# Kernel optimization log

Measured on AMD Instinct MI355X. Metric: run time of the kernel, lower is better.

Reference implementation:

```python
import jax, jax.numpy as jnp
import numpy as np

BITS = 4
PACK = 32 // BITS  # 8 nibbles per int32
MASK = (1 << BITS) - 1  # 0xF, maxq for 4-bit


def _unpack_rows(q):
    # q: [K//PACK, N] int32, nibbles packed along the input (row) dim
    shifts = (jnp.arange(PACK, dtype=jnp.int32) * BITS)
    vals = (q[:, None, :] >> shifts[None, :, None]) & MASK  # [K//PACK, PACK, N]
    return vals.reshape(q.shape[0] * PACK, q.shape[1])      # [K, N]


def _unpack_cols(q):
    # q: [1, N//PACK] int32, nibbles packed along the output (col) dim
    shifts = (jnp.arange(PACK, dtype=jnp.int32) * BITS)
    vals = (q[:, :, None] >> shifts[None, None, :]) & MASK  # [1, N//PACK, PACK]
    return vals.reshape(q.shape[0], q.shape[1] * PACK)       # [1, N]


def setup_inputs() -> dict:
    key = jax.random.key(0)
    k1, k2, k3, k4 = jax.random.split(key, 4)
    M, K, N = 4096, 4096, 11008
    x = jax.random.normal(k1, (M, K), dtype=jnp.float16)
    qweight = jax.random.randint(k2, (K // PACK, N), jnp.iinfo(jnp.int32).min,
                                 jnp.iinfo(jnp.int32).max, dtype=jnp.int32)
    qzeros = jax.random.randint(k3, (1, N // PACK), jnp.iinfo(jnp.int32).min,
                                jnp.iinfo(jnp.int32).max, dtype=jnp.int32)
    # realistic small positive per-channel scales
    scales = (jax.random.uniform(k4, (1, N), dtype=jnp.float32) * 0.01 + 1e-3).astype(jnp.float16)
    return {"x": x, "qweight": qweight, "qzeros": qzeros, "scales": scales}


def reference(x, qweight, qzeros, scales):
    # GPTQ/exllama 4-bit dequant: w = scale * (q - (zero + 1)), single group
    wq = _unpack_rows(qweight)                      # [K, N] int32 in [0, 15]
    zeros = _unpack_cols(qzeros) + 1                # [1, N] int32
    w = (wq - zeros).astype(jnp.float16) * scales   # [K, N] fp16
    out = jnp.dot(x, w)                             # [M, N] fp16 GEMM
    return out
```

## Files before the change

kernel.cpp:

```cpp
#include <hip/hip_runtime.h>
#include <stdint.h>

#define M_DIM 4096
#define K_DIM 4096
#define N_DIM 11008

typedef _Float16 half2v __attribute__((ext_vector_type(2)));
typedef _Float16 half8  __attribute__((ext_vector_type(8)));
typedef float    f32x4  __attribute__((ext_vector_type(4)));

__device__ __forceinline__ unsigned int pkrtz_bits(float a, float b) {
  typedef __fp16 fp16x2 __attribute__((ext_vector_type(2)));
  union { fp16x2 h; unsigned int u; } c;
  c.h = __builtin_amdgcn_cvt_pkrtz(a, b);
  return c.u;
}

__device__ __forceinline__ half8 pack8(float4 lo, float4 hi) {
  union { unsigned int u[4]; half8 v; } r;
  r.u[0] = pkrtz_bits(lo.x, hi.x);
  r.u[1] = pkrtz_bits(lo.y, hi.y);
  r.u[2] = pkrtz_bits(lo.z, hi.z);
  r.u[3] = pkrtz_bits(lo.w, hi.w);
  return r.v;
}

__global__ __launch_bounds__(256) void convert_x(const float* __restrict__ X,
                                                 _Float16* __restrict__ X16) {
  size_t g = (size_t)blockIdx.x * 256 + threadIdx.x;
  const float4* p = (const float4*)(X + g * 8);
  float4 lo = p[0], hi = p[1];
  *(half8*)(X16 + g * 8) = pack8(lo, hi);
}

__device__ __forceinline__ half8 unpack8(unsigned int q, half2v zoff) {
  union { unsigned int u; half2v h; } t0, t1, t2, t3;
  t0.u = (q & 0x000F000Fu) | 0x64006400u;
  t1.u = ((q >> 4) & 0x000F000Fu) | 0x64006400u;
  t2.u = ((q >> 8) & 0x000F000Fu) | 0x64006400u;
  t3.u = ((q >> 12) & 0x000F000Fu) | 0x64006400u;
  union { half2v h[4]; half8 v; } r;
  r.h[0] = t0.h - zoff;
  r.h[1] = t1.h - zoff;
  r.h[2] = t2.h - zoff;
  r.h[3] = t3.h - zoff;
  return r.v;
}

__device__ __forceinline__ void stage16(const void* g, void* l) {
  __builtin_amdgcn_global_load_lds((__attribute__((address_space(1))) unsigned int*)g,
                                   (__attribute__((address_space(3))) unsigned int*)l,
                                   16, 0, 0);
}

__global__ __launch_bounds__(256, 3) void gptq_gemm(
    const _Float16* __restrict__ X16,
    const int* __restrict__ QW,
    const int* __restrict__ QZ,
    const float* __restrict__ SC,
    float* __restrict__ OUT) {
  const int tid  = threadIdx.x;
  const int lane = tid & 63;
  const int wave = tid >> 6;
  const int wr   = wave >> 1;
  const int wc   = wave & 1;
  const int quad = lane >> 4;
  const int l16  = lane & 15;
  const int bx = blockIdx.x;
  const int by = blockIdx.y;

  __shared__ __align__(16) _Float16 ldsA[2 * 1024 * 8];

  const _Float16* gA = X16 + (size_t)(by * 128 + (tid & 127)) * K_DIM + (tid >> 7) * 8;
  _Float16* lA = ldsA + (size_t)tid * 8;

  const int* qp = QW + (size_t)quad * N_DIM + bx * 128 + wc * 64 + l16;

  half2v zoff[4];
  float sc[4];
#pragma unroll
  for (int nt = 0; nt < 4; ++nt) {
    int n = bx * 128 + wc * 64 + nt * 16 + l16;
    int z = (QZ[n >> 3] >> ((n & 7) * 4)) & 15;
    union { unsigned int u; half2v h; } zc;
    unsigned int zb = 0x6400u + (unsigned int)(z + 1);
    zc.u = (zb << 16) | zb;
    zoff[nt] = zc.h;
    sc[nt] = SC[n];
  }

  f32x4 acc[4][4] = {};

#pragma unroll
  for (int i = 0; i < 4; ++i)
    stage16(gA + i * 16, lA + i * 2048);
  int q[2][4];
#pragma unroll
  for (int s = 0; s < 2; ++s)
#pragma unroll
    for (int nt = 0; nt < 4; ++nt)
      q[s][nt] = qp[(s * 4) * N_DIM + nt * 16];
  __syncthreads();

  int p = 0;
  for (int ks = 0; ks < 64; ++ks) {
    int nq[2][4];
    if (ks < 63) {
      gA += 64;
      qp += 8 * N_DIM;
      _Float16* lb = ldsA + (p ^ 1) * 8192 + (size_t)tid * 8;
#pragma unroll
      for (int i = 0; i < 4; ++i)
        stage16(gA + i * 16, lb + i * 2048);
#pragma unroll
      for (int s = 0; s < 2; ++s)
#pragma unroll
        for (int nt = 0; nt < 4; ++nt)
          nq[s][nt] = qp[(s * 4) * N_DIM + nt * 16];
    }

    const _Float16* base = ldsA + p * 8192;
#pragma unroll
    for (int s = 0; s < 2; ++s) {
      half8 a[4];
#pragma unroll
      for (int mt = 0; mt < 4; ++mt)
        a[mt] = *(const half8*)(base + ((s * 4 + quad) * 128 + wr * 64 + mt * 16 + l16) * 8);
      half8 b[4];
#pragma unroll
      for (int nt = 0; nt < 4; ++nt)
        b[nt] = unpack8((unsigned int)q[s][nt], zoff[nt]);
#pragma unroll
      for (int mt = 0; mt < 4; ++mt)
#pragma unroll
        for (int nt = 0; nt < 4; ++nt)
          acc[mt][nt] = __builtin_amdgcn_mfma_f32_16x16x32_f16(a[mt], b[nt], acc[mt][nt], 0, 0, 0);
    }
    __syncthreads();
    if (ks < 63) {
#pragma unroll
      for (int s = 0; s < 2; ++s)
#pragma unroll
        for (int nt = 0; nt < 4; ++nt)
          q[s][nt] = nq[s][nt];
    }
    p ^= 1;
  }

#pragma unroll
  for (int mt = 0; mt < 4; ++mt) {
    int mbase = by * 128 + wr * 64 + mt * 16 + quad * 4;
#pragma unroll
    for (int nt = 0; nt < 4; ++nt) {
      int n = bx * 128 + wc * 64 + nt * 16 + l16;
      float s = sc[nt];
#pragma unroll
      for (int pp = 0; pp < 4; ++pp)
        OUT[(size_t)(mbase + pp) * N_DIM + n] = acc[mt][nt][pp] * s;
    }
  }
}

extern "C" void kernel_launch(void* const* d_in, const int* in_sizes, int n_in,
                              void* d_out, int out_size, void* d_ws, size_t ws_size,
                              hipStream_t stream) {
  const float* X  = (const float*)d_in[0];
  const int* QW   = (const int*)d_in[1];
  const int* QZ   = (const int*)d_in[2];
  const float* SC = (const float*)d_in[3];
  float* OUT      = (float*)d_out;
  _Float16* X16   = (_Float16*)d_ws;

  convert_x<<<dim3((M_DIM * (size_t)K_DIM / 8) / 256), 256, 0, stream>>>(X, X16);
  dim3 grid(N_DIM / 128, M_DIM / 128);
  gptq_gemm<<<grid, 256, 0, stream>>>(X16, QW, QZ, SC, OUT);
}
```

Before: 662.2 us.

## Triple-buffer A tiles in LDS with partial vmcnt waits and MFMA priority

Moves from a double-buffered LDS pipeline to three buffers with prefetch depth two. Each iteration issues loads for A and qweight two stages ahead, then waits with a partial s_waitcnt vmcnt(12) before a raw s_barrier instead of a full __syncthreads drain, so global loads stay in flight across iterations. It also raises wave priority around the MFMA block and adds sched_barrier fences to pin the instruction order. This adds LDS use (48KB per block, which may cut occupancy from 3 blocks per CU) and more live registers. The hand-counted vmcnt must match the actual number of outstanding loads, or the kernel will read stale data.

```diff
diff --git a/kernel.cpp b/kernel.cpp
--- a/kernel.cpp
+++ b/kernel.cpp
@@ -8,6 +8,8 @@
 typedef _Float16 half2v __attribute__((ext_vector_type(2)));
 typedef _Float16 half8  __attribute__((ext_vector_type(8)));
 typedef float    f32x4  __attribute__((ext_vector_type(4)));
+
+#define SCHED_FENCE() __builtin_amdgcn_sched_barrier(0)
 
 __device__ __forceinline__ unsigned int pkrtz_bits(float a, float b) {
   typedef __fp16 fp16x2 __attribute__((ext_vector_type(2)));
@@ -69,10 +71,10 @@
   const int bx = blockIdx.x;
   const int by = blockIdx.y;
 
-  __shared__ __align__(16) _Float16 ldsA[2 * 1024 * 8];
+  __shared__ __align__(16) _Float16 ldsA[3 * 1024 * 8];
 
   const _Float16* gA = X16 + (size_t)(by * 128 + (tid & 127)) * K_DIM + (tid >> 7) * 8;
-  _Float16* lA = ldsA + (size_t)tid * 8;
+  _Float16* lw = ldsA + (size_t)tid * 8;
 
   const int* qp = QW + (size_t)quad * N_DIM + bx * 128 + wc * 64 + l16;
 
@@ -91,24 +93,40 @@
 
   f32x4 acc[4][4] = {};
 
+  int q0[2][4], q1[2][4];
 #pragma unroll
   for (int i = 0; i < 4; ++i)
-    stage16(gA + i * 16, lA + i * 2048);
-  int q[2][4];
+    stage16(gA + i * 16, lw + i * 2048);
+  SCHED_FENCE();
 #pragma unroll
   for (int s = 0; s < 2; ++s)
 #pragma unroll
     for (int nt = 0; nt < 4; ++nt)
-      q[s][nt] = qp[(s * 4) * N_DIM + nt * 16];
-  __syncthreads();
-
-  int p = 0;
+      q0[s][nt] = qp[(s * 4) * N_DIM + nt * 16];
+  SCHED_FENCE();
+  gA += 64;
+  qp += 8 * N_DIM;
+#pragma unroll
+  for (int i = 0; i < 4; ++i)
+    stage16(gA + i * 16, lw + 8192 + i * 2048);
+  SCHED_FENCE();
+#pragma unroll
+  for (int s = 0; s < 2; ++s)
+#pragma unroll
+    for (int nt = 0; nt < 4; ++nt)
+      q1[s][nt] = qp[(s * 4) * N_DIM + nt * 16];
+  SCHED_FENCE();
+  asm volatile("s_waitcnt vmcnt(12)" ::: "memory");
+  __builtin_amdgcn_s_barrier();
+
+  int rb = 0;
+  int wb = 2;
   for (int ks = 0; ks < 64; ++ks) {
     int nq[2][4];
-    if (ks < 63) {
+    if (ks < 62) {
       gA += 64;
       qp += 8 * N_DIM;
-      _Float16* lb = ldsA + (p ^ 1) * 8192 + (size_t)tid * 8;
+      _Float16* lb = ldsA + wb * 8192 + (size_t)tid * 8;
 #pragma unroll
       for (int i = 0; i < 4; ++i)
         stage16(gA + i * 16, lb + i * 2048);
@@ -117,9 +135,10 @@
 #pragma unroll
         for (int nt = 0; nt < 4; ++nt)
           nq[s][nt] = qp[(s * 4) * N_DIM + nt * 16];
-    }
-
-    const _Float16* base = ldsA + p * 8192;
+      SCHED_FENCE();
+    }
+
+    const _Float16* base = ldsA + rb * 8192;
 #pragma unroll
     for (int s = 0; s < 2; ++s) {
       half8 a[4];
@@ -129,22 +148,34 @@
       half8 b[4];
 #pragma unroll
       for (int nt = 0; nt < 4; ++nt)
-        b[nt] = unpack8((unsigned int)q[s][nt], zoff[nt]);
+        b[nt] = unpack8((unsigned int)q0[s][nt], zoff[nt]);
+      __builtin_amdgcn_s_setprio(1);
 #pragma unroll
       for (int mt = 0; mt < 4; ++mt)
 #pragma unroll
         for (int nt = 0; nt < 4; ++nt)
           acc[mt][nt] = __builtin_amdgcn_mfma_f32_16x16x32_f16(a[mt], b[nt], acc[mt][nt], 0, 0, 0);
-    }
-    __syncthreads();
+      __builtin_amdgcn_s_setprio(0);
+    }
+
+#pragma unroll
+    for (int s = 0; s < 2; ++s)
+#pragma unroll
+      for (int nt = 0; nt < 4; ++nt) {
+        q0[s][nt] = q1[s][nt];
+        if (ks < 62) q1[s][nt] = nq[s][nt];
+      }
+    rb = (rb == 2) ? 0 : rb + 1;
+    wb = (wb == 2) ? 0 : wb + 1;
+
     if (ks < 63) {
-#pragma unroll
-      for (int s = 0; s < 2; ++s)
-#pragma unroll
-        for (int nt = 0; nt < 4; ++nt)
-          q[s][nt] = nq[s][nt];
-    }
-    p ^= 1;
+      SCHED_FENCE();
+      if (ks < 62)
+        asm volatile("s_waitcnt vmcnt(12)" ::: "memory");
+      else
+        asm volatile("s_waitcnt vmcnt(0)" ::: "memory");
+      __builtin_amdgcn_s_barrier();
+    }
   }
 
 #pragma unroll
```

Measured after the change: 643.5 us. -2.8%, faster.

## Triple-buffer LDS and weight loads with manual vmcnt waits and MFMA priority

Applied to the files above, without the earlier changes.

The K loop moves from a double-buffered LDS pipeline to a three-stage ring, unrolled by three so buffer indices are compile-time constants. Prefetches now run two stages ahead. __syncthreads is replaced with explicit s_waitcnt vmcnt(12) plus s_barrier, so the newest stage's loads can stay in flight. It also adds sched_barrier fences and s_setprio around the MFMA blocks to shape instruction ordering. The cost is 50% more LDS, which may limit occupancy, and reliance on hand-counted vmcnt values being correct.

```diff
diff --git a/kernel.cpp b/kernel.cpp
--- a/kernel.cpp
+++ b/kernel.cpp
@@ -8,6 +8,8 @@
 typedef _Float16 half2v __attribute__((ext_vector_type(2)));
 typedef _Float16 half8  __attribute__((ext_vector_type(8)));
 typedef float    f32x4  __attribute__((ext_vector_type(4)));
+
+#define SCHED_FENCE() __builtin_amdgcn_sched_barrier(0)
 
 __device__ __forceinline__ unsigned int pkrtz_bits(float a, float b) {
   typedef __fp16 fp16x2 __attribute__((ext_vector_type(2)));
@@ -69,10 +71,10 @@
   const int bx = blockIdx.x;
   const int by = blockIdx.y;
 
-  __shared__ __align__(16) _Float16 ldsA[2 * 1024 * 8];
+  __shared__ __align__(16) _Float16 ldsA[3 * 1024 * 8];
 
   const _Float16* gA = X16 + (size_t)(by * 128 + (tid & 127)) * K_DIM + (tid >> 7) * 8;
-  _Float16* lA = ldsA + (size_t)tid * 8;
+  _Float16* lw = ldsA + (size_t)tid * 8;
 
   const int* qp = QW + (size_t)quad * N_DIM + bx * 128 + wc * 64 + l16;
 
@@ -90,36 +92,88 @@
   }
 
   f32x4 acc[4][4] = {};
+  int q[3][2][4];
 
 #pragma unroll
   for (int i = 0; i < 4; ++i)
-    stage16(gA + i * 16, lA + i * 2048);
-  int q[2][4];
+    stage16(gA + i * 16, lw + i * 2048);
+  SCHED_FENCE();
 #pragma unroll
   for (int s = 0; s < 2; ++s)
 #pragma unroll
     for (int nt = 0; nt < 4; ++nt)
-      q[s][nt] = qp[(s * 4) * N_DIM + nt * 16];
-  __syncthreads();
-
-  int p = 0;
-  for (int ks = 0; ks < 64; ++ks) {
-    int nq[2][4];
-    if (ks < 63) {
-      gA += 64;
-      qp += 8 * N_DIM;
-      _Float16* lb = ldsA + (p ^ 1) * 8192 + (size_t)tid * 8;
-#pragma unroll
-      for (int i = 0; i < 4; ++i)
-        stage16(gA + i * 16, lb + i * 2048);
-#pragma unroll
-      for (int s = 0; s < 2; ++s)
-#pragma unroll
-        for (int nt = 0; nt < 4; ++nt)
-          nq[s][nt] = qp[(s * 4) * N_DIM + nt * 16];
-    }
-
-    const _Float16* base = ldsA + p * 8192;
+      q[0][s][nt] = qp[(s * 4) * N_DIM + nt * 16];
+  SCHED_FENCE();
+  gA += 64;
+  qp += 8 * N_DIM;
+#pragma unroll
+  for (int i = 0; i < 4; ++i)
+    stage16(gA + i * 16, lw + 8192 + i * 2048);
+  SCHED_FENCE();
+#pragma unroll
+  for (int s = 0; s < 2; ++s)
+#pragma unroll
+    for (int nt = 0; nt < 4; ++nt)
+      q[1][s][nt] = qp[(s * 4) * N_DIM + nt * 16];
+  SCHED_FENCE();
+  asm volatile("s_waitcnt vmcnt(12)" ::: "memory");
+  __builtin_amdgcn_s_barrier();
+
+#define STAGE_BODY(KS, RB, WB)                                                \
+  {                                                                           \
+    const int ks = (KS);                                                      \
+    if (ks < 62) {                                                            \
+      gA += 64;                                                               \
+      qp += 8 * N_DIM;                                                        \
+      _Float16* lb = ldsA + (WB) * 8192 + (size_t)tid * 8;                    \
+      _Pragma("unroll")                                                       \
+      for (int i = 0; i < 4; ++i)                                             \
+        stage16(gA + i * 16, lb + i * 2048);                                  \
+      _Pragma("unroll")                                                       \
+      for (int s = 0; s < 2; ++s)                                             \
+        _Pragma("unroll")                                                     \
+        for (int nt = 0; nt < 4; ++nt)                                        \
+          q[WB][s][nt] = qp[(s * 4) * N_DIM + nt * 16];                       \
+      SCHED_FENCE();                                                          \
+    }                                                                         \
+    const _Float16* base = ldsA + (RB) * 8192;                                \
+    _Pragma("unroll")                                                         \
+    for (int s = 0; s < 2; ++s) {                                             \
+      half8 a[4];                                                             \
+      _Pragma("unroll")                                                       \
+      for (int mt = 0; mt < 4; ++mt)                                          \
+        a[mt] = *(const half8*)(base +                                        \
+                 ((s * 4 + quad) * 128 + wr * 64 + mt * 16 + l16) * 8);       \
+      half8 b[4];                                                             \
+      _Pragma("unroll")                                                       \
+      for (int nt = 0; nt < 4; ++nt)                                          \
+        b[nt] = unpack8((unsigned int)q[RB][s][nt], zoff[nt]);                \
+      __builtin_amdgcn_s_setprio(1);                                          \
+      _Pragma("unroll")                                                       \
+      for (int mt = 0; mt < 4; ++mt)                                          \
+        _Pragma("unroll")                                                     \
+        for (int nt = 0; nt < 4; ++nt)                                        \
+          acc[mt][nt] = __builtin_amdgcn_mfma_f32_16x16x32_f16(               \
+              a[mt], b[nt], acc[mt][nt], 0, 0, 0);                            \
+      __builtin_amdgcn_s_setprio(0);                                          \
+    }                                                                         \
+    SCHED_FENCE();                                                            \
+    if (ks < 62)                                                              \
+      asm volatile("s_waitcnt vmcnt(12)" ::: "memory");                       \
+    else                                                                      \
+      asm volatile("s_waitcnt vmcnt(0)" ::: "memory");                        \
+    __builtin_amdgcn_s_barrier();                                             \
+  }
+
+  for (int it = 0; it < 21; ++it) {
+    STAGE_BODY(it * 3 + 0, 0, 2)
+    STAGE_BODY(it * 3 + 1, 1, 0)
+    STAGE_BODY(it * 3 + 2, 2, 1)
+  }
+#undef STAGE_BODY
+
+  {
+    const _Float16* base = ldsA;
 #pragma unroll
     for (int s = 0; s < 2; ++s) {
       half8 a[4];
@@ -129,22 +183,15 @@
       half8 b[4];
 #pragma unroll
       for (int nt = 0; nt < 4; ++nt)
-        b[nt] = unpack8((unsigned int)q[s][nt], zoff[nt]);
+        b[nt] = unpack8((unsigned int)q[0][s][nt], zoff[nt]);
+      __builtin_amdgcn_s_setprio(1);
 #pragma unroll
       for (int mt = 0; mt < 4; ++mt)
 #pragma unroll
         for (int nt = 0; nt < 4; ++nt)
           acc[mt][nt] = __builtin_amdgcn_mfma_f32_16x16x32_f16(a[mt], b[nt], acc[mt][nt], 0, 0, 0);
+      __builtin_amdgcn_s_setprio(0);
     }
-    __syncthreads();
-    if (ks < 63) {
-#pragma unroll
-      for (int s = 0; s < 2; ++s)
-#pragma unroll
-        for (int nt = 0; nt < 4; ++nt)
-          q[s][nt] = nq[s][nt];
-    }
-    p ^= 1;
   }
 
 #pragma unroll
```

New measurement: 663.8 us. About the same (+0.2%).

## Use 256x256 tiles with 32x32 MFMA and triple-buffered phased pipeline

Applied to the files above, without the earlier changes.

Enlarges the block tile to 256x256 with 512 threads and switches to 32x32x16 MFMA instructions. A/B staging becomes a three-buffer pipeline split into per-k-chunk phases with explicit barriers, waitcnts and MFMA priority boosts. The aim is more operand reuse per loaded and dequantized weight and better hiding of global-load latency. The 96KB LDS footprint and high accumulator register count may limit occupancy to one block per CU.

```diff
diff --git a/kernel.cpp b/kernel.cpp
--- a/kernel.cpp
+++ b/kernel.cpp
@@ -7,7 +7,9 @@
 
 typedef _Float16 half2v __attribute__((ext_vector_type(2)));
 typedef _Float16 half8  __attribute__((ext_vector_type(8)));
-typedef float    f32x4  __attribute__((ext_vector_type(4)));
+typedef float    f32x16 __attribute__((ext_vector_type(16)));
+
+#define SCHED_FENCE() __builtin_amdgcn_sched_barrier(0)
 
 __device__ __forceinline__ unsigned int pkrtz_bits(float a, float b) {
   typedef __fp16 fp16x2 __attribute__((ext_vector_type(2)));
@@ -53,7 +55,7 @@
                                    16, 0, 0);
 }
 
-__global__ __launch_bounds__(256, 3) void gptq_gemm(
+__global__ __launch_bounds__(512, 2) void gptq_gemm(
     const _Float16* __restrict__ X16,
     const int* __restrict__ QW,
     const int* __restrict__ QZ,
@@ -62,25 +64,25 @@
   const int tid  = threadIdx.x;
   const int lane = tid & 63;
   const int wave = tid >> 6;
-  const int wr   = wave >> 1;
-  const int wc   = wave & 1;
-  const int quad = lane >> 4;
-  const int l16  = lane & 15;
+  const int wr   = wave >> 2;
+  const int wn   = wave & 3;
+  const int l32  = lane & 31;
+  const int kh   = lane >> 5;
   const int bx = blockIdx.x;
   const int by = blockIdx.y;
 
-  __shared__ __align__(16) _Float16 ldsA[2 * 1024 * 8];
-
-  const _Float16* gA = X16 + (size_t)(by * 128 + (tid & 127)) * K_DIM + (tid >> 7) * 8;
-  _Float16* lA = ldsA + (size_t)tid * 8;
-
-  const int* qp = QW + (size_t)quad * N_DIM + bx * 128 + wc * 64 + l16;
-
-  half2v zoff[4];
-  float sc[4];
-#pragma unroll
-  for (int nt = 0; nt < 4; ++nt) {
-    int n = bx * 128 + wc * 64 + nt * 16 + l16;
+  __shared__ __align__(16) _Float16 ldsA[3 * 16384];
+
+  const _Float16* gA = X16 + (size_t)(by * 256 + (tid & 255)) * K_DIM + (tid >> 8) * 8;
+  _Float16* lwt = ldsA + (size_t)tid * 8;
+
+  const int* qB = QW + (size_t)kh * N_DIM + bx * 256 + wn * 64 + l32;
+
+  half2v zoff[2];
+  float sc[2];
+#pragma unroll
+  for (int nt = 0; nt < 2; ++nt) {
+    int n = bx * 256 + wn * 64 + nt * 32 + l32;
     int z = (QZ[n >> 3] >> ((n & 7) * 4)) & 15;
     union { unsigned int u; half2v h; } zc;
     unsigned int zb = 0x6400u + (unsigned int)(z + 1);
@@ -89,74 +91,120 @@
     sc[nt] = SC[n];
   }
 
-  f32x4 acc[4][4] = {};
+  f32x16 acc[4][2] = {};
+  int q[3][4][2];
 
 #pragma unroll
   for (int i = 0; i < 4; ++i)
-    stage16(gA + i * 16, lA + i * 2048);
-  int q[2][4];
-#pragma unroll
-  for (int s = 0; s < 2; ++s)
-#pragma unroll
-    for (int nt = 0; nt < 4; ++nt)
-      q[s][nt] = qp[(s * 4) * N_DIM + nt * 16];
-  __syncthreads();
-
-  int p = 0;
-  for (int ks = 0; ks < 64; ++ks) {
-    int nq[2][4];
-    if (ks < 63) {
-      gA += 64;
-      qp += 8 * N_DIM;
-      _Float16* lb = ldsA + (p ^ 1) * 8192 + (size_t)tid * 8;
-#pragma unroll
-      for (int i = 0; i < 4; ++i)
-        stage16(gA + i * 16, lb + i * 2048);
-#pragma unroll
-      for (int s = 0; s < 2; ++s)
-#pragma unroll
-        for (int nt = 0; nt < 4; ++nt)
-          nq[s][nt] = qp[(s * 4) * N_DIM + nt * 16];
-    }
-
-    const _Float16* base = ldsA + p * 8192;
-#pragma unroll
-    for (int s = 0; s < 2; ++s) {
-      half8 a[4];
-#pragma unroll
-      for (int mt = 0; mt < 4; ++mt)
-        a[mt] = *(const half8*)(base + ((s * 4 + quad) * 128 + wr * 64 + mt * 16 + l16) * 8);
-      half8 b[4];
-#pragma unroll
-      for (int nt = 0; nt < 4; ++nt)
-        b[nt] = unpack8((unsigned int)q[s][nt], zoff[nt]);
-#pragma unroll
-      for (int mt = 0; mt < 4; ++mt)
-#pragma unroll
-        for (int nt = 0; nt < 4; ++nt)
-          acc[mt][nt] = __builtin_amdgcn_mfma_f32_16x16x32_f16(a[mt], b[nt], acc[mt][nt], 0, 0, 0);
-    }
-    __syncthreads();
-    if (ks < 63) {
-#pragma unroll
-      for (int s = 0; s < 2; ++s)
-#pragma unroll
-        for (int nt = 0; nt < 4; ++nt)
-          q[s][nt] = nq[s][nt];
-    }
-    p ^= 1;
+    stage16(gA + i * 16, lwt + i * 4096);
+#pragma unroll
+  for (int p = 0; p < 4; ++p)
+#pragma unroll
+    for (int nt = 0; nt < 2; ++nt)
+      q[0][p][nt] = qB[(size_t)(p * 2) * N_DIM + nt * 32];
+  SCHED_FENCE();
+#pragma unroll
+  for (int i = 0; i < 4; ++i)
+    stage16(gA + 64 + i * 16, lwt + 16384 + i * 4096);
+#pragma unroll
+  for (int p = 0; p < 4; ++p)
+#pragma unroll
+    for (int nt = 0; nt < 2; ++nt)
+      q[1][p][nt] = qB[(size_t)(8 + p * 2) * N_DIM + nt * 32];
+  SCHED_FENCE();
+  gA += 64;
+  qB += (size_t)8 * N_DIM;
+  asm volatile("s_waitcnt vmcnt(12)" ::: "memory");
+  __builtin_amdgcn_s_barrier();
+
+#define PHASE(P, RB, WB, LT62, KS62)                                          \
+  {                                                                           \
+    const _Float16* ab = ldsA + (RB) * 16384 +                                \
+        (size_t)(((P) * 2 + kh) * 256 + wr * 128 + l32) * 8;                  \
+    half8 a0 = *(const half8*)(ab + 0 * 256);                                 \
+    half8 a1 = *(const half8*)(ab + 1 * 256);                                 \
+    half8 a2 = *(const half8*)(ab + 2 * 256);                                 \
+    half8 a3 = *(const half8*)(ab + 3 * 256);                                 \
+    if (LT62) {                                                               \
+      stage16(gA + (P) * 16, lwt + (WB) * 16384 + (P) * 4096);                \
+      q[WB][P][0] = qB[(size_t)((P) * 2) * N_DIM];                            \
+      q[WB][P][1] = qB[(size_t)((P) * 2) * N_DIM + 32];                       \
+      SCHED_FENCE();                                                          \
+    }                                                                         \
+    __builtin_amdgcn_s_barrier();                                             \
+    asm volatile("s_waitcnt lgkmcnt(0)" ::: "memory");                        \
+    {                                                                         \
+      half8 b0 = unpack8((unsigned int)q[RB][(P)][0], zoff[0]);               \
+      half8 b1 = unpack8((unsigned int)q[RB][(P)][1], zoff[1]);               \
+      __builtin_amdgcn_s_setprio(1);                                          \
+      acc[0][0] = __builtin_amdgcn_mfma_f32_32x32x16_f16(a0, b0, acc[0][0], 0, 0, 0); \
+      acc[0][1] = __builtin_amdgcn_mfma_f32_32x32x16_f16(a0, b1, acc[0][1], 0, 0, 0); \
+      acc[1][0] = __builtin_amdgcn_mfma_f32_32x32x16_f16(a1, b0, acc[1][0], 0, 0, 0); \
+      acc[1][1] = __builtin_amdgcn_mfma_f32_32x32x16_f16(a1, b1, acc[1][1], 0, 0, 0); \
+      acc[2][0] = __builtin_amdgcn_mfma_f32_32x32x16_f16(a2, b0, acc[2][0], 0, 0, 0); \
+      acc[2][1] = __builtin_amdgcn_mfma_f32_32x32x16_f16(a2, b1, acc[2][1], 0, 0, 0); \
+      acc[3][0] = __builtin_amdgcn_mfma_f32_32x32x16_f16(a3, b0, acc[3][0], 0, 0, 0); \
+      acc[3][1] = __builtin_amdgcn_mfma_f32_32x32x16_f16(a3, b1, acc[3][1], 0, 0, 0); \
+      __builtin_amdgcn_s_setprio(0);                                          \
+    }                                                                         \
+    if ((P) == 3) {                                                           \
+      if (KS62) asm volatile("s_waitcnt vmcnt(0)" ::: "memory");              \
+      else      asm volatile("s_waitcnt vmcnt(12)" ::: "memory");             \
+    }                                                                         \
+    __builtin_amdgcn_s_barrier();                                             \
+  }
+
+#define STAGE(KS, RB, WB)                                                     \
+  {                                                                           \
+    const int ks_ = (KS);                                                     \
+    const bool lt62 = (ks_ < 62);                                             \
+    const bool k62  = (ks_ == 62);                                            \
+    if (lt62) { gA += 64; qB += (size_t)8 * N_DIM; }                          \
+    PHASE(0, RB, WB, lt62, k62)                                               \
+    PHASE(1, RB, WB, lt62, k62)                                               \
+    PHASE(2, RB, WB, lt62, k62)                                               \
+    PHASE(3, RB, WB, lt62, k62)                                               \
+  }
+
+  for (int it = 0; it < 21; ++it) {
+    STAGE(it * 3 + 0, 0, 2)
+    STAGE(it * 3 + 1, 1, 0)
+    STAGE(it * 3 + 2, 2, 1)
+  }
+#undef STAGE
+#undef PHASE
+
+#pragma unroll
+  for (int p = 0; p < 4; ++p) {
+    const _Float16* ab = ldsA + (size_t)((p * 2 + kh) * 256 + wr * 128 + l32) * 8;
+    half8 a0 = *(const half8*)(ab + 0 * 256);
+    half8 a1 = *(const half8*)(ab + 1 * 256);
+    half8 a2 = *(const half8*)(ab + 2 * 256);
+    half8 a3 = *(const half8*)(ab + 3 * 256);
+    half8 b0 = unpack8((unsigned int)q[0][p][0], zoff[0]);
+    half8 b1 = unpack8((unsigned int)q[0][p][1], zoff[1]);
+    acc[0][0] = __builtin_amdgcn_mfma_f32_32x32x16_f16(a0, b0, acc[0][0], 0, 0, 0);
+    acc[0][1] = __builtin_amdgcn_mfma_f32_32x32x16_f16(a0, b1, acc[0][1], 0, 0, 0);
+    acc[1][0] = __builtin_amdgcn_mfma_f32_32x32x16_f16(a1, b0, acc[1][0], 0, 0, 0);
+    acc[1][1] = __builtin_amdgcn_mfma_f32_32x32x16_f16(a1, b1, acc[1][1], 0, 0, 0);
+    acc[2][0] = __builtin_amdgcn_mfma_f32_32x32x16_f16(a2, b0, acc[2][0], 0, 0, 0);
+    acc[2][1] = __builtin_amdgcn_mfma_f32_32x32x16_f16(a2, b1, acc[2][1], 0, 0, 0);
+    acc[3][0] = __builtin_amdgcn_mfma_f32_32x32x16_f16(a3, b0, acc[3][0], 0, 0, 0);
+    acc[3][1] = __builtin_amdgcn_mfma_f32_32x32x16_f16(a3, b1, acc[3][1], 0, 0, 0);
   }
 
 #pragma unroll
   for (int mt = 0; mt < 4; ++mt) {
-    int mbase = by * 128 + wr * 64 + mt * 16 + quad * 4;
-#pragma unroll
-    for (int nt = 0; nt < 4; ++nt) {
-      int n = bx * 128 + wc * 64 + nt * 16 + l16;
-      float s = sc[nt];
-#pragma unroll
-      for (int pp = 0; pp < 4; ++pp)
-        OUT[(size_t)(mbase + pp) * N_DIM + n] = acc[mt][nt][pp] * s;
+#pragma unroll
+    for (int nt = 0; nt < 2; ++nt) {
+      const int n = bx * 256 + wn * 64 + nt * 32 + l32;
+      const float s = sc[nt];
+      const size_t mb = (size_t)(by * 256 + wr * 128 + mt * 32 + kh * 4);
+#pragma unroll
+      for (int r = 0; r < 16; ++r) {
+        const int row = (r & 3) + 8 * (r >> 2);
+        OUT[(mb + row) * N_DIM + n] = acc[mt][nt][r] * s;
+      }
     }
   }
 }
@@ -172,6 +220,6 @@
   _Float16* X16   = (_Float16*)d_ws;
 
   convert_x<<<dim3((M_DIM * (size_t)K_DIM / 8) / 256), 256, 0, stream>>>(X, X16);
-  dim3 grid(N_DIM / 128, M_DIM / 128);
-  gptq_gemm<<<grid, 256, 0, stream>>>(X16, QW, QZ, SC, OUT);
-}
+  dim3 grid(N_DIM / 256, M_DIM / 256);
+  gptq_gemm<<<grid, 512, 0, stream>>>(X16, QW, QZ, SC, OUT);
+}
```

After: 676.7 us. +2.2%, slower.
